# Optimization experiments

Measured on AMD Instinct MI355X. Metric: run time of the kernel, lower is better.

The kernel has to match this reference:

```python
import jax, jax.numpy as jnp
import numpy as np

K, N, E, D = 4, 2048, 4096, 128
BETA = 0.6
EPS = 0.01           # epsilon in hard-sigmoid gating
LAM = 0.05           # lambda_schedule
TC0, TCMAX = 0.3, 0.7
COS_EPS = 1e-8       # F.cosine_similarity eps
MAX_SCORED_EDGES = 500
EDGE_DENSITY = 0.008


def setup_inputs() -> dict:
    key = jax.random.key(0)
    ks = jax.random.split(key, 8)
    s = 0.02
    H = (jax.random.uniform(ks[0], (K, N, E)) < EDGE_DENSITY).astype(jnp.float32)
    X = jax.random.normal(ks[1], (N, D), jnp.float32)
    return dict(
        H=H, X=X, epoch=50,
        mlp_w1=jax.random.normal(ks[2], (K, D, D), jnp.float32) * s,
        mlp_b1=jnp.zeros((K, D), jnp.float32),
        mlp_w2=jax.random.normal(ks[3], (K, D, D), jnp.float32) * s,
        mlp_b2=jnp.zeros((K, D), jnp.float32),
        comp_W=jax.random.normal(ks[4], (K, D, D), jnp.float32) * 0.01,
        att_w1=jax.random.normal(ks[5], (K, D, D // 2), jnp.float32) * s,
        att_b1=jnp.zeros((K, D // 2), jnp.float32),
        att_w2=jax.random.normal(ks[6], (K, D // 2, 1), jnp.float32) * s,
        att_b2=jnp.zeros((K, 1), jnp.float32),
    )


def reference(H, X, epoch, mlp_w1, mlp_b1, mlp_w2, mlp_b2, comp_W,
              att_w1, att_b1, att_w2, att_b2):
    # ---- component level (Eq. 4, batched over K) ----
    h1 = jax.nn.relu(jnp.einsum('nd,kdh->knh', X, mlp_w1) + mlp_b1[:, None, :])
    Xk = jnp.einsum('knh,khe->kne', h1, mlp_w2) + mlp_b2[:, None, :]        # [K,N,D]
    a1 = jax.nn.relu(jnp.einsum('knd,kdh->knh', Xk, att_w1) + att_b1[:, None, :])
    att = jax.nn.sigmoid(jnp.einsum('knh,kho->kno', a1, att_w2) + att_b2[:, None, :])
    S_att = att.mean(axis=(1, 2))                                            # [K]
    frob = jnp.sqrt((comp_W ** 2).sum(axis=(1, 2)))                          # ||W_k||_F
    featn = jnp.sqrt((Xk ** 2).sum(axis=(1, 2)))                             # ||MLP(X_k)||_2 (Frobenius)
    imp = BETA * frob * featn + (1.0 - BETA) * S_att
    pi_c = jax.nn.softmax(imp)
    theta_c = TC0 + (1.0 - jnp.exp(-LAM * epoch)) * (TCMAX - TC0)            # Eq. 3 schedule
    gates = jnp.clip((pi_c - theta_c) / EPS + 0.5, 0.0, 1.0)                 # hard sigmoid
    # K_min = max(1, int(0.1*K)) = 1 -> force top-1 gate open
    keep = jax.nn.one_hot(jnp.argmax(gates), K, dtype=gates.dtype)
    gates = jnp.maximum(gates, keep)

    xnorm = jnp.linalg.norm(X, axis=1)                                       # [N]
    xhat = X / jnp.maximum(xnorm, COS_EPS)[:, None]
    er = jnp.arange(E)
    eye = jnp.eye(N, dtype=bool)

    Hp_l, eg_l, npi_l = [], [], []
    for k in range(K):  # small fixed component count
        Hk = H[k]
        mask = Hk > 0                                                        # [N,E]
        cnt = mask.sum(axis=0)                                               # nodes per hyperedge
        order = jnp.cumsum(mask, axis=0)
        i = jnp.argmax(mask, axis=0)                                         # first incident node
        j = jnp.argmax(mask & (order == 2), axis=0)                          # second incident node
        cos = (xhat[i] * xhat[j]).sum(-1)                                    # [E]
        A = Hk[i, er] * Hk[j, er]                                            # A_ij per edge
        # torch loop: only first 500 edges scored; <2-node edges get 0.1; rest 0
        imp_e = jnp.where(er < MAX_SCORED_EDGES,
                          jnp.where(cnt >= 2, A * cos, 0.1), 0.0)
        pi_e = jax.nn.softmax(imp_e)
        theta_e = jnp.minimum(theta_c, pi_e.mean() + jnp.std(pi_e, ddof=1))  # torch.std unbiased
        eg = jnp.clip((pi_e - theta_e) / EPS + 0.5, 0.0, 1.0)
        eg = jnp.where((eg.sum() < 1.0) & (er == jnp.argmax(pi_e)), 1.0, eg)
        eg_eff = jnp.where(gates[k] > 0.5, eg, jnp.ones_like(eg))
        Hp = Hk * gates[k] * eg_eff[None, :]                                 # pruned incidence

        # ---- node level (Eq. 7) on pruned graph ----
        B = (Hp > 0).astype(Hk.dtype)
        Adj = ((B @ B.T) > 0) & (~eye)                                       # shared-hyperedge neighbors
        degf = Adj.sum(axis=1).astype(Hk.dtype)
        nsum = Adj.astype(Hk.dtype) @ xhat                                   # sum of neighbor unit vecs
        avg = jnp.where(degf > 0, (xhat * nsum).sum(-1) / jnp.maximum(degf, 1.0), 0.0)
        npi = jax.nn.softmax(avg * xnorm)
        Hp_l.append(Hp); eg_l.append(eg); npi_l.append(npi)

    return (jnp.stack(Hp_l), gates, jnp.stack(eg_l), jnp.stack(npi_l))
```

## Files before the change

### kernel.cpp

```cpp
#include <hip/hip_runtime.h>
#include <math.h>

#define KCOMP 4
#define NN 2048
#define EE 4096
#define DD 128
#define MAXNE 96
#define MAXSE 500
#define BETA_C 0.6f
#define EPS_G 0.01f
#define LAM_S 0.05f
#define TC0_C 0.3f
#define TCMAX_C 0.7f
#define COS_EPS_C 1e-8f

typedef float vf4 __attribute__((ext_vector_type(4)));

static const size_t OFF_XHAT   = 0;
static const size_t OFF_XNORM  = 1048576;
static const size_t OFF_SCAL   = 1056768;
static const size_t OFF_NCNT   = 1057024;
static const size_t OFF_EMASK  = 1089792;
static const size_t OFF_NELIST = 5284096;
static const size_t OFF_IMPE   = 6856960;
static const size_t OFF_EGS    = 6865152;
static const size_t OFF_Z      = 6930688;
static const size_t OFF_FEAT   = 6963456;
static const size_t OFF_ATT    = 6965504;
static const size_t OFF_FROB   = 6967552;

__global__ __launch_bounds__(1024) void k_d1(
    const float4* __restrict__ H4, unsigned* __restrict__ emask,
    const float* __restrict__ X, float* __restrict__ xhat, float* __restrict__ xnorm,
    const float* __restrict__ w1, const float* __restrict__ b1,
    const float* __restrict__ w2, const float* __restrict__ b2,
    const float* __restrict__ aw1, const float* __restrict__ ab1,
    const float* __restrict__ aw2, const float* __restrict__ ab2,
    const float4* __restrict__ compW4, int* __restrict__ ncnt,
    unsigned short* __restrict__ nelist,
    float* __restrict__ featA, float* __restrict__ attA, float* __restrict__ frobA) {
  __shared__ float smem[16416];
  int b = blockIdx.x, t = threadIdx.x;
  if (b < 128) {
    int k = b >> 5;
    int bx = b & 31;
    float* Xs  = smem;
    float* H1s = smem + 8192;
    float* A1s = H1s;
    float* red = smem + 16384;
    int n0 = bx * 64;
    for (int i = t; i < 64 * 128; i += 1024) Xs[i] = X[(size_t)n0 * 128 + i];
    __syncthreads();

    int h = t & 127, g = t >> 7;
    const float* W1 = w1 + (size_t)k * 128 * 128;
    float acc[8];
    {
      float bb = b1[k * 128 + h];
#pragma unroll
      for (int rr = 0; rr < 8; ++rr) acc[rr] = bb;
    }
    for (int d = 0; d < 128; d += 4) {
      float wa = W1[(d + 0) * 128 + h];
      float wb = W1[(d + 1) * 128 + h];
      float wc = W1[(d + 2) * 128 + h];
      float wd2 = W1[(d + 3) * 128 + h];
#pragma unroll
      for (int rr = 0; rr < 8; ++rr) {
        float4 x = *(const float4*)&Xs[(g * 8 + rr) * 128 + d];
        acc[rr] = fmaf(x.x, wa, acc[rr]); acc[rr] = fmaf(x.y, wb, acc[rr]);
        acc[rr] = fmaf(x.z, wc, acc[rr]); acc[rr] = fmaf(x.w, wd2, acc[rr]);
      }
    }
#pragma unroll
    for (int rr = 0; rr < 8; ++rr) H1s[(g * 8 + rr) * 128 + h] = fmaxf(acc[rr], 0.f);
    __syncthreads();

    const float* W2 = w2 + (size_t)k * 128 * 128;
    {
      float bb = b2[k * 128 + h];
#pragma unroll
      for (int rr = 0; rr < 8; ++rr) acc[rr] = bb;
    }
    for (int d = 0; d < 128; d += 4) {
      float wa = W2[(d + 0) * 128 + h];
      float wb = W2[(d + 1) * 128 + h];
      float wc = W2[(d + 2) * 128 + h];
      float wd2 = W2[(d + 3) * 128 + h];
#pragma unroll
      for (int rr = 0; rr < 8; ++rr) {
        float4 x = *(const float4*)&H1s[(g * 8 + rr) * 128 + d];
        acc[rr] = fmaf(x.x, wa, acc[rr]); acc[rr] = fmaf(x.y, wb, acc[rr]);
        acc[rr] = fmaf(x.z, wc, acc[rr]); acc[rr] = fmaf(x.w, wd2, acc[rr]);
      }
    }
    float fpart = 0.f;
    __syncthreads();
#pragma unroll
    for (int rr = 0; rr < 8; ++rr) {
      Xs[(g * 8 + rr) * 128 + h] = acc[rr];
      fpart = fmaf(acc[rr], acc[rr], fpart);
    }
    __syncthreads();

    int h2 = t & 63, g4 = t >> 6;
    const float* AW1 = aw1 + (size_t)k * 128 * 64;
    float a4[4];
    {
      float ab = ab1[k * 64 + h2];
#pragma unroll
      for (int q = 0; q < 4; ++q) a4[q] = ab;
    }
    for (int d = 0; d < 128; d += 4) {
      float wa = AW1[(d + 0) * 64 + h2];
      float wb = AW1[(d + 1) * 64 + h2];
      float wc = AW1[(d + 2) * 64 + h2];
      float wd2 = AW1[(d + 3) * 64 + h2];
#pragma unroll
      for (int q = 0; q < 4; ++q) {
        float4 x = *(const float4*)&Xs[(g4 * 4 + q) * 128 + d];
        a4[q] = fmaf(x.x, wa, a4[q]); a4[q] = fmaf(x.y, wb, a4[q]);
        a4[q] = fmaf(x.z, wc, a4[q]); a4[q] = fmaf(x.w, wd2, a4[q]);
      }
    }
    __syncthreads();
#pragma unroll
    for (int q = 0; q < 4; ++q) A1s[(g4 * 4 + q) * 64 + h2] = fmaxf(a4[q], 0.f);
    __syncthreads();

    float attsum = 0.f;
    if (t < 64) {
      const float* AW2 = aw2 + (size_t)k * 64;
      float a = ab2[k];
      for (int d = 0; d < 64; d += 4) {
        float4 av = *(const float4*)&A1s[t * 64 + d];
        a = fmaf(av.x, AW2[d + 0], a);
        a = fmaf(av.y, AW2[d + 1], a);
        a = fmaf(av.z, AW2[d + 2], a);
        a = fmaf(av.w, AW2[d + 3], a);
      }
      attsum = 1.f / (1.f + expf(-a));
    }
    for (int o = 32; o > 0; o >>= 1) {
      fpart  += __shfl_xor(fpart, o, 64);
      attsum += __shfl_xor(attsum, o, 64);
    }
    int wv = t >> 6, ln = t & 63;
    if (ln == 0) { red[wv] = fpart; red[16 + wv] = attsum; }
    __syncthreads();
    if (t == 0) {
      float fs = 0.f, as = 0.f;
#pragma unroll
      for (int i = 0; i < 16; i++) { fs += red[i]; as += red[16 + i]; }
      featA[k * 128 + bx] = fs;
      attA[k * 128 + bx]  = as;
    }
    return;
  }
  if (b < 384) {
    unsigned* lds = (unsigned*)smem;
    int sb = b - 128;
    int k = sb >> 6;
    int rem = sb & 63;
    int ch_super = rem >> 4;
    int e4_super = rem & 15;
    int chi = t >> 6;
    int e4i = t & 63;
    int ch = ch_super * 16 + chi;
    int e4 = e4_super * 64 + e4i;
    int n0 = ch * 32;
    const float4* p = H4 + ((size_t)(k * NN + n0)) * (EE / 4) + e4;
    unsigned w0 = 0, w1b = 0, w2b = 0, w3 = 0;
    for (int rb = 0; rb < 32; rb += 8) {
      float4 v[8];
#pragma unroll
      for (int u = 0; u < 8; ++u) v[u] = p[(size_t)(rb + u) * (EE / 4)];
#pragma unroll
      for (int u = 0; u < 8; ++u) {
        unsigned bit = 1u << (rb + u);
        w0  |= (v[u].x > 0.f) ? bit : 0u;
        w1b |= (v[u].y > 0.f) ? bit : 0u;
        w2b |= (v[u].z > 0.f) ? bit : 0u;
        w3  |= (v[u].w > 0.f) ? bit : 0u;
      }
    }
    int el = e4i * 4;
    lds[(el + 0) * 17 + chi] = w0;
    lds[(el + 1) * 17 + chi] = w1b;
    lds[(el + 2) * 17 + chi] = w2b;
    lds[(el + 3) * 17 + chi] = w3;
    {
      int ebase = e4 * 4;
      unsigned ws[4] = {w0, w1b, w2b, w3};
#pragma unroll
      for (int j = 0; j < 4; ++j) {
        unsigned wd = ws[j];
        while (wd) {
          int bit = __builtin_ctz(wd); wd &= wd - 1;
          int node = n0 + bit;
          int slot = atomicAdd(&ncnt[k * NN + node], 1);
          if (slot < MAXNE)
            nelist[((size_t)(k * NN + node)) * MAXNE + slot] =
                (unsigned short)(ebase + j);
        }
      }
    }
    __syncthreads();
    int e_base = e4_super * 256;
    int wi = t & 15;
    int eo = t >> 4;
#pragma unroll
    for (int it = 0; it < 4; ++it) {
      int e_local = it * 64 + eo;
      emask[((size_t)(k * EE) + e_base + e_local) * 64 + ch_super * 16 + wi] =
          lds[e_local * 17 + wi];
    }
    return;
  }
  if (b < 512) {
    int xb = b - 384;
    int node = xb * 16 + (t >> 6);
    int lane = t & 63;
    float2 v = ((const float2*)X)[(size_t)node * 64 + lane];
    float ss = v.x * v.x + v.y * v.y;
    for (int o = 32; o > 0; o >>= 1) ss += __shfl_xor(ss, o, 64);
    float nrm = sqrtf(ss);
    float den = fmaxf(nrm, COS_EPS_C);
    if (lane == 0) xnorm[node] = nrm;
    float2 o2; o2.x = v.x / den; o2.y = v.y / den;
    ((float2*)xhat)[(size_t)node * 64 + lane] = o2;
    return;
  }
  {
    int fb = b - 512;
    int k = fb >> 2, idx = fb & 3;
    float* red = smem;
    float4 v = compW4[(size_t)k * 4096 + idx * 1024 + t];
    float s = v.x * v.x + v.y * v.y + v.z * v.z + v.w * v.w;
    for (int o = 32; o > 0; o >>= 1) s += __shfl_xor(s, o, 64);
    int wv = t >> 6, ln = t & 63;
    if (ln == 0) red[wv] = s;
    __syncthreads();
    if (t == 0) {
      float fs = 0.f;
#pragma unroll
      for (int i = 0; i < 16; i++) fs += red[i];
      frobA[k * 4 + idx] = fs;
    }
  }
}

__global__ void k_d2(const unsigned* __restrict__ emask, const float* __restrict__ xhat,
                     float* __restrict__ impE) {
  int t = threadIdx.x;
  int k = blockIdx.y;
  int bx = blockIdx.x;
  int e = bx * 4 + (t >> 6);
  int lane = t & 63;
  unsigned w = emask[((size_t)(k * EE) + e) * 64 + lane];
  int pc = __popc(w);
  for (int o = 32; o > 0; o >>= 1) pc += __shfl_xor(pc, o, 64);
  float impv = 0.1f;
  if (pc >= 2) {
    unsigned l1 = w ? (unsigned)((lane << 5) + __builtin_ctz(w)) : 0xffffffffu;
    unsigned wr = w & (w - 1);
    unsigned l2 = wr ? (unsigned)((lane << 5) + __builtin_ctz(wr)) : 0xffffffffu;
    unsigned g1 = l1;
    for (int o = 32; o > 0; o >>= 1) {
      unsigned x = (unsigned)__shfl_xor((int)g1, o, 64);
      g1 = g1 < x ? g1 : x;
    }
    unsigned cand = (l1 == g1) ? l2 : l1;
    unsigned g2 = cand;
    for (int o = 32; o > 0; o >>= 1) {
      unsigned x = (unsigned)__shfl_xor((int)g2, o, 64);
      g2 = g2 < x ? g2 : x;
    }
    float2 xi = ((const float2*)xhat)[(size_t)g1 * 64 + lane];
    float2 xj = ((const float2*)xhat)[(size_t)g2 * 64 + lane];
    float d = xi.x * xj.x + xi.y * xj.y;
    for (int o = 32; o > 0; o >>= 1) d += __shfl_xor(d, o, 64);
    impv = d;
  }
  if (lane == 0) impE[k * 512 + e] = impv;
}

__device__ __forceinline__ float blockReduceSum16(float v, float* red, int t) {
  for (int o = 32; o > 0; o >>= 1) v += __shfl_xor(v, o, 64);
  __syncthreads();
  if ((t & 63) == 0) red[t >> 6] = v;
  __syncthreads();
  float s = red[0];
#pragma unroll
  for (int i = 1; i < 16; i++) s += red[i];
  return s;
}

__global__ void k_edgegate(const float* __restrict__ impE,
                           const float* __restrict__ featA, const float* __restrict__ attA,
                           const float* __restrict__ frobA, float* __restrict__ scal,
                           const int* __restrict__ epoch, float* __restrict__ out_gates,
                           float* __restrict__ egscaled, float* __restrict__ out_eg) {
  __shared__ float red[16];
  __shared__ int redi[16];
  __shared__ float imps[KCOMP];
  int k = blockIdx.x;
  int t = threadIdx.x;
  int wv0 = t >> 6, ln0 = t & 63;
  if (wv0 < KCOMP) {
    float pf = (ln0 < 32) ? featA[wv0 * 128 + ln0] : 0.f;
    float pa = (ln0 < 32) ? attA[wv0 * 128 + ln0] : 0.f;
    float pr = (ln0 < 4) ? frobA[wv0 * 4 + ln0] : 0.f;
    for (int o = 32; o > 0; o >>= 1) {
      pf += __shfl_xor(pf, o, 64);
      pa += __shfl_xor(pa, o, 64);
      pr += __shfl_xor(pr, o, 64);
    }
    if (ln0 == 0)
      imps[wv0] = BETA_C * sqrtf(pr) * sqrtf(pf) + (1.f - BETA_C) * (pa / (float)NN);
  }
  __syncthreads();
  float gates[KCOMP];
  float tc;
  {
    float mx = imps[0];
    for (int kk = 1; kk < KCOMP; kk++) mx = fmaxf(mx, imps[kk]);
    float ex[KCOMP], ssum = 0.f;
    for (int kk = 0; kk < KCOMP; kk++) { ex[kk] = expf(imps[kk] - mx); ssum += ex[kk]; }
    tc = TC0_C + (1.f - expf(-LAM_S * (float)epoch[0])) * (TCMAX_C - TC0_C);
    for (int kk = 0; kk < KCOMP; kk++) {
      float pi = ex[kk] / ssum;
      gates[kk] = fminf(fmaxf((pi - tc) / EPS_G + 0.5f, 0.f), 1.f);
    }
    int am = 0; float bv2 = gates[0];
    for (int kk = 1; kk < KCOMP; kk++) if (gates[kk] > bv2) { bv2 = gates[kk]; am = kk; }
    gates[am] = fmaxf(gates[am], 1.f);
  }
  if (t == 0) {
    scal[12 + k] = gates[k];
    if (k == 0) for (int kk = 0; kk < KCOMP; kk++) out_gates[kk] = gates[kk];
  }
  float imp[4];
#pragma unroll
  for (int j = 0; j < 4; j++) {
    int e = t + j * 1024;
    imp[j] = (e < MAXSE) ? impE[k * 512 + e] : 0.f;
  }
  float m = fmaxf(fmaxf(imp[0], imp[1]), fmaxf(imp[2], imp[3]));
  for (int o = 32; o > 0; o >>= 1) m = fmaxf(m, __shfl_xor(m, o, 64));
  __syncthreads();
  if ((t & 63) == 0) red[t >> 6] = m;
  __syncthreads();
  m = red[0];
#pragma unroll
  for (int i = 1; i < 16; i++) m = fmaxf(m, red[i]);
  float p[4], psum = 0.f;
#pragma unroll
  for (int j = 0; j < 4; j++) { p[j] = expf(imp[j] - m); psum += p[j]; }
  float S = blockReduceSum16(psum, red, t);
  float pi[4], tot = 0.f;
#pragma unroll
  for (int j = 0; j < 4; j++) { pi[j] = p[j] / S; tot += pi[j]; }
  float T = blockReduceSum16(tot, red, t);
  float mean = T / (float)EE;
  float devs = 0.f;
#pragma unroll
  for (int j = 0; j < 4; j++) { float d = pi[j] - mean; devs = fmaf(d, d, devs); }
  float V = blockReduceSum16(devs, red, t);
  float stdv = sqrtf(V / (float)(EE - 1));
  float theta = fminf(tc, mean + stdv);
  float eg[4], egsum = 0.f;
#pragma unroll
  for (int j = 0; j < 4; j++) {
    eg[j] = fminf(fmaxf((pi[j] - theta) / EPS_G + 0.5f, 0.f), 1.f);
    egsum += eg[j];
  }
  float EGS = blockReduceSum16(egsum, red, t);
  float bv = -1e30f; int bi = 0x7fffffff;
#pragma unroll
  for (int j = 0; j < 4; j++) if (pi[j] > bv) { bv = pi[j]; bi = t + j * 1024; }
  for (int o = 32; o > 0; o >>= 1) {
    float ov = __shfl_xor(bv, o, 64); int oi = __shfl_xor(bi, o, 64);
    if (ov > bv || (ov == bv && oi < bi)) { bv = ov; bi = oi; }
  }
  __syncthreads();
  if ((t & 63) == 0) { red[t >> 6] = bv; redi[t >> 6] = bi; }
  __syncthreads();
  float abv = red[0]; int abi = redi[0];
#pragma unroll
  for (int i = 1; i < 16; i++) {
    float ov = red[i]; int oi = redi[i];
    if (ov > abv || (ov == abv && oi < abi)) { abv = ov; abi = oi; }
  }
  float g = gates[k];
#pragma unroll
  for (int j = 0; j < 4; j++) {
    int e = t + j * 1024;
    float egv = eg[j];
    if (EGS < 1.f && e == abi) egv = 1.f;
    out_eg[(size_t)k * EE + e] = egv;
    float eff = (g > 0.5f) ? egv : 1.f;
    egscaled[k * EE + e] = g * eff;
  }
}

__global__ void k_hprow(const unsigned* __restrict__ emask,
                        const int* __restrict__ ncnt, const unsigned short* __restrict__ nelist,
                        const float* __restrict__ egs, const float* __restrict__ scal,
                        const float* __restrict__ xhat, const float* __restrict__ xnorm,
                        float* __restrict__ out, float* __restrict__ z) {
  __shared__ unsigned short elds[MAXNE];
  __shared__ float evals[MAXNE];
  __shared__ unsigned wpart[4][64];
  __shared__ unsigned short list[2048];
  __shared__ int cnt_s;
  __shared__ float sred[4];
  int k = blockIdx.y, n = blockIdx.x, t = threadIdx.x;
  float g = scal[12 + k];
  float* orow = out + ((size_t)(k * NN + n)) * EE;
  vf4* o4 = (vf4*)orow;
  vf4 z4 = {0.f, 0.f, 0.f, 0.f};
  if (g <= 0.f) {
#pragma unroll
    for (int i = 0; i < 4; i++) __builtin_nontemporal_store(z4, &o4[t + i * 256]);
    if (t == 0) z[k * NN + n] = 0.f;
    return;
  }
  int ec = ncnt[k * NN + n]; if (ec > MAXNE) ec = MAXNE;
  if (t == 0) cnt_s = 0;
  if (t < ec) {
    int e = nelist[((size_t)(k * NN + n)) * MAXNE + t];
    elds[t] = (unsigned short)e;
    evals[t] = egs[k * EE + e];
  }
#pragma unroll
  for (int i = 0; i < 4; i++) __builtin_nontemporal_store(z4, &o4[t + i * 256]);
  __syncthreads();
  if (t < ec) orow[elds[t]] = evals[t];
  int lane = t & 63, wv = t >> 6;
  unsigned acc = 0;
  for (int it = wv; it < ec; it += 4) {
    if (evals[it] > 0.f) acc |= emask[((size_t)(k * EE) + elds[it]) * 64 + lane];
  }
  wpart[wv][lane] = acc;
  __syncthreads();
  if (t < 64) {
    unsigned w = wpart[0][t] | wpart[1][t] | wpart[2][t] | wpart[3][t];
    if (t == (n >> 5)) w &= ~(1u << (n & 31));
    int c = __popc(w);
    if (c > 0) {
      int base = atomicAdd(&cnt_s, c);
      while (w) {
        int b = __builtin_ctz(w); w &= w - 1;
        list[base++] = (unsigned short)((t << 5) + b);
      }
    }
  }
  __syncthreads();
  int cnt = cnt_s;
  if (cnt == 0) { if (t == 0) z[k * NN + n] = 0.f; return; }
  int fc = lane & 31, hh = lane >> 5;
  float4 xn4 = ((const float4*)xhat)[(size_t)n * 32 + fc];
  float a = 0.f;
#pragma unroll 4
  for (int it = wv * 2 + hh; it < cnt; it += 8) {
    int m = (int)list[it];
    float4 xm = ((const float4*)xhat)[(size_t)m * 32 + fc];
    a += xn4.x * xm.x + xn4.y * xm.y + xn4.z * xm.z + xn4.w * xm.w;
  }
  for (int o = 32; o > 0; o >>= 1) a += __shfl_xor(a, o, 64);
  if (lane == 0) sred[wv] = a;
  __syncthreads();
  if (t == 0) {
    float s = sred[0] + sred[1] + sred[2] + sred[3];
    z[k * NN + n] = (s / (float)cnt) * xnorm[n];
  }
}

__global__ void k_npi(const float* __restrict__ z, float* __restrict__ out_npi) {
  __shared__ float red[4];
  int k = blockIdx.x, t = threadIdx.x;
  float v[8]; float m = -1e30f;
#pragma unroll
  for (int j = 0; j < 8; j++) { v[j] = z[k * NN + t + j * 256]; m = fmaxf(m, v[j]); }
  for (int o = 32; o > 0; o >>= 1) m = fmaxf(m, __shfl_xor(m, o, 64));
  if ((t & 63) == 0) red[t >> 6] = m;
  __syncthreads();
  m = fmaxf(fmaxf(red[0], red[1]), fmaxf(red[2], red[3]));
  __syncthreads();
  float pe[8]; float s = 0.f;
#pragma unroll
  for (int j = 0; j < 8; j++) { pe[j] = expf(v[j] - m); s += pe[j]; }
  for (int o = 32; o > 0; o >>= 1) s += __shfl_xor(s, o, 64);
  if ((t & 63) == 0) red[t >> 6] = s;
  __syncthreads();
  s = red[0] + red[1] + red[2] + red[3];
#pragma unroll
  for (int j = 0; j < 8; j++) out_npi[k * NN + t + j * 256] = pe[j] / s;
}

extern "C" void kernel_launch(void* const* d_in, const int* in_sizes, int n_in,
                              void* d_out, int out_size, void* d_ws, size_t ws_size,
                              hipStream_t stream) {
  const float* H     = (const float*)d_in[0];
  const float* X     = (const float*)d_in[1];
  const int*   epoch = (const int*)d_in[2];
  const float* w1    = (const float*)d_in[3];
  const float* b1    = (const float*)d_in[4];
  const float* w2    = (const float*)d_in[5];
  const float* b2    = (const float*)d_in[6];
  const float* compW = (const float*)d_in[7];
  const float* aw1   = (const float*)d_in[8];
  const float* ab1   = (const float*)d_in[9];
  const float* aw2   = (const float*)d_in[10];
  const float* ab2   = (const float*)d_in[11];

  char* ws = (char*)d_ws;
  float* xhat  = (float*)(ws + OFF_XHAT);
  float* xnorm = (float*)(ws + OFF_XNORM);
  float* scal  = (float*)(ws + OFF_SCAL);
  int*   ncnt  = (int*)(ws + OFF_NCNT);
  unsigned* emask = (unsigned*)(ws + OFF_EMASK);
  unsigned short* nelist = (unsigned short*)(ws + OFF_NELIST);
  float* impE  = (float*)(ws + OFF_IMPE);
  float* egs   = (float*)(ws + OFF_EGS);
  float* zbuf  = (float*)(ws + OFF_Z);
  float* featA = (float*)(ws + OFF_FEAT);
  float* attA  = (float*)(ws + OFF_ATT);
  float* frobA = (float*)(ws + OFF_FROB);

  float* out       = (float*)d_out;
  float* out_gates = out + (size_t)KCOMP * NN * EE;
  float* out_eg    = out_gates + KCOMP;
  float* out_npi   = out_eg + (size_t)KCOMP * EE;

  hipMemsetAsync(ncnt, 0, (size_t)KCOMP * NN * sizeof(int), stream);
  k_d1<<<528, 1024, 0, stream>>>((const float4*)H, emask, X, xhat, xnorm,
                                 w1, b1, w2, b2, aw1, ab1, aw2, ab2,
                                 (const float4*)compW, ncnt, nelist, featA, attA, frobA);
  k_d2<<<dim3(125, KCOMP), 256, 0, stream>>>(emask, xhat, impE);
  k_edgegate<<<KCOMP, 1024, 0, stream>>>(impE, featA, attA, frobA, scal, epoch,
                                         out_gates, egs, out_eg);
  k_hprow<<<dim3(NN, KCOMP), 256, 0, stream>>>(emask, ncnt, nelist, egs, scal, xhat, xnorm,
                                               out, zbuf);
  k_npi<<<KCOMP, 256, 0, stream>>>(zbuf, out_npi);
}
```

Before: 299.2 us.

## Register-tile MLP matmuls in k_d1 and fold edge scoring into k_edgegate

The per-component MLP and attention matmuls in k_d1 now use 2x4 and 1x4 register tiles with float4 weight and shared-memory loads, in place of one output column per thread. This raises arithmetic per load and cuts LDS traffic. The separate k_d2 launch that scored the first 500 hyperedges is removed, and that work now runs at the start of k_edgegate into shared memory. This saves one kernel launch and a global round trip, but the scoring now runs on only 4 blocks instead of 500.

```diff
diff --git a/kernel.cpp b/kernel.cpp
--- a/kernel.cpp
+++ b/kernel.cpp
@@ -22,7 +22,6 @@
 static const size_t OFF_NCNT   = 1057024;
 static const size_t OFF_EMASK  = 1089792;
 static const size_t OFF_NELIST = 5284096;
-static const size_t OFF_IMPE   = 6856960;
 static const size_t OFF_EGS    = 6865152;
 static const size_t OFF_Z      = 6930688;
 static const size_t OFF_FEAT   = 6963456;
@@ -52,80 +51,122 @@
     for (int i = t; i < 64 * 128; i += 1024) Xs[i] = X[(size_t)n0 * 128 + i];
     __syncthreads();
 
-    int h = t & 127, g = t >> 7;
+    int hq = t & 31, rq = t >> 5;
+    int h0 = hq * 4;
+    float acc0[4], acc1[4];
+    {
+      float4 bb = *(const float4*)&b1[k * 128 + h0];
+      acc0[0] = bb.x; acc0[1] = bb.y; acc0[2] = bb.z; acc0[3] = bb.w;
+      acc1[0] = bb.x; acc1[1] = bb.y; acc1[2] = bb.z; acc1[3] = bb.w;
+    }
     const float* W1 = w1 + (size_t)k * 128 * 128;
-    float acc[8];
-    {
-      float bb = b1[k * 128 + h];
-#pragma unroll
-      for (int rr = 0; rr < 8; ++rr) acc[rr] = bb;
-    }
     for (int d = 0; d < 128; d += 4) {
-      float wa = W1[(d + 0) * 128 + h];
-      float wb = W1[(d + 1) * 128 + h];
-      float wc = W1[(d + 2) * 128 + h];
-      float wd2 = W1[(d + 3) * 128 + h];
-#pragma unroll
-      for (int rr = 0; rr < 8; ++rr) {
-        float4 x = *(const float4*)&Xs[(g * 8 + rr) * 128 + d];
-        acc[rr] = fmaf(x.x, wa, acc[rr]); acc[rr] = fmaf(x.y, wb, acc[rr]);
-        acc[rr] = fmaf(x.z, wc, acc[rr]); acc[rr] = fmaf(x.w, wd2, acc[rr]);
-      }
-    }
-#pragma unroll
-    for (int rr = 0; rr < 8; ++rr) H1s[(g * 8 + rr) * 128 + h] = fmaxf(acc[rr], 0.f);
-    __syncthreads();
-
+      float wm[4][4], xa0[4], xa1[4];
+#pragma unroll
+      for (int i = 0; i < 4; ++i) {
+        float4 w = *(const float4*)&W1[(d + i) * 128 + h0];
+        wm[i][0] = w.x; wm[i][1] = w.y; wm[i][2] = w.z; wm[i][3] = w.w;
+      }
+      {
+        float4 x0 = *(const float4*)&Xs[(rq * 2 + 0) * 128 + d];
+        float4 x1 = *(const float4*)&Xs[(rq * 2 + 1) * 128 + d];
+        xa0[0] = x0.x; xa0[1] = x0.y; xa0[2] = x0.z; xa0[3] = x0.w;
+        xa1[0] = x1.x; xa1[1] = x1.y; xa1[2] = x1.z; xa1[3] = x1.w;
+      }
+#pragma unroll
+      for (int j = 0; j < 4; ++j) {
+#pragma unroll
+        for (int i = 0; i < 4; ++i) acc0[j] = fmaf(xa0[i], wm[i][j], acc0[j]);
+#pragma unroll
+        for (int i = 0; i < 4; ++i) acc1[j] = fmaf(xa1[i], wm[i][j], acc1[j]);
+      }
+    }
+    {
+      float4 s0, s1;
+      s0.x = fmaxf(acc0[0], 0.f); s0.y = fmaxf(acc0[1], 0.f);
+      s0.z = fmaxf(acc0[2], 0.f); s0.w = fmaxf(acc0[3], 0.f);
+      s1.x = fmaxf(acc1[0], 0.f); s1.y = fmaxf(acc1[1], 0.f);
+      s1.z = fmaxf(acc1[2], 0.f); s1.w = fmaxf(acc1[3], 0.f);
+      *(float4*)&H1s[(rq * 2 + 0) * 128 + h0] = s0;
+      *(float4*)&H1s[(rq * 2 + 1) * 128 + h0] = s1;
+    }
+    __syncthreads();
+
+    {
+      float4 bb = *(const float4*)&b2[k * 128 + h0];
+      acc0[0] = bb.x; acc0[1] = bb.y; acc0[2] = bb.z; acc0[3] = bb.w;
+      acc1[0] = bb.x; acc1[1] = bb.y; acc1[2] = bb.z; acc1[3] = bb.w;
+    }
     const float* W2 = w2 + (size_t)k * 128 * 128;
-    {
-      float bb = b2[k * 128 + h];
-#pragma unroll
-      for (int rr = 0; rr < 8; ++rr) acc[rr] = bb;
-    }
     for (int d = 0; d < 128; d += 4) {
-      float wa = W2[(d + 0) * 128 + h];
-      float wb = W2[(d + 1) * 128 + h];
-      float wc = W2[(d + 2) * 128 + h];
-      float wd2 = W2[(d + 3) * 128 + h];
-#pragma unroll
-      for (int rr = 0; rr < 8; ++rr) {
-        float4 x = *(const float4*)&H1s[(g * 8 + rr) * 128 + d];
-        acc[rr] = fmaf(x.x, wa, acc[rr]); acc[rr] = fmaf(x.y, wb, acc[rr]);
-        acc[rr] = fmaf(x.z, wc, acc[rr]); acc[rr] = fmaf(x.w, wd2, acc[rr]);
+      float wm[4][4], xa0[4], xa1[4];
+#pragma unroll
+      for (int i = 0; i < 4; ++i) {
+        float4 w = *(const float4*)&W2[(d + i) * 128 + h0];
+        wm[i][0] = w.x; wm[i][1] = w.y; wm[i][2] = w.z; wm[i][3] = w.w;
+      }
+      {
+        float4 x0 = *(const float4*)&H1s[(rq * 2 + 0) * 128 + d];
+        float4 x1 = *(const float4*)&H1s[(rq * 2 + 1) * 128 + d];
+        xa0[0] = x0.x; xa0[1] = x0.y; xa0[2] = x0.z; xa0[3] = x0.w;
+        xa1[0] = x1.x; xa1[1] = x1.y; xa1[2] = x1.z; xa1[3] = x1.w;
+      }
+#pragma unroll
+      for (int j = 0; j < 4; ++j) {
+#pragma unroll
+        for (int i = 0; i < 4; ++i) acc0[j] = fmaf(xa0[i], wm[i][j], acc0[j]);
+#pragma unroll
+        for (int i = 0; i < 4; ++i) acc1[j] = fmaf(xa1[i], wm[i][j], acc1[j]);
       }
     }
     float fpart = 0.f;
     __syncthreads();
-#pragma unroll
-    for (int rr = 0; rr < 8; ++rr) {
-      Xs[(g * 8 + rr) * 128 + h] = acc[rr];
-      fpart = fmaf(acc[rr], acc[rr], fpart);
-    }
-    __syncthreads();
-
-    int h2 = t & 63, g4 = t >> 6;
+    {
+      float4 s0, s1;
+      s0.x = acc0[0]; s0.y = acc0[1]; s0.z = acc0[2]; s0.w = acc0[3];
+      s1.x = acc1[0]; s1.y = acc1[1]; s1.z = acc1[2]; s1.w = acc1[3];
+      *(float4*)&Xs[(rq * 2 + 0) * 128 + h0] = s0;
+      *(float4*)&Xs[(rq * 2 + 1) * 128 + h0] = s1;
+#pragma unroll
+      for (int j = 0; j < 4; ++j) {
+        fpart = fmaf(acc0[j], acc0[j], fpart);
+        fpart = fmaf(acc1[j], acc1[j], fpart);
+      }
+    }
+    __syncthreads();
+
+    int hq3 = t & 15, rq3 = t >> 4;
+    int h0a = hq3 * 4;
     const float* AW1 = aw1 + (size_t)k * 128 * 64;
     float a4[4];
     {
-      float ab = ab1[k * 64 + h2];
-#pragma unroll
-      for (int q = 0; q < 4; ++q) a4[q] = ab;
+      float4 ab = *(const float4*)&ab1[k * 64 + h0a];
+      a4[0] = ab.x; a4[1] = ab.y; a4[2] = ab.z; a4[3] = ab.w;
     }
     for (int d = 0; d < 128; d += 4) {
-      float wa = AW1[(d + 0) * 64 + h2];
-      float wb = AW1[(d + 1) * 64 + h2];
-      float wc = AW1[(d + 2) * 64 + h2];
-      float wd2 = AW1[(d + 3) * 64 + h2];
-#pragma unroll
-      for (int q = 0; q < 4; ++q) {
-        float4 x = *(const float4*)&Xs[(g4 * 4 + q) * 128 + d];
-        a4[q] = fmaf(x.x, wa, a4[q]); a4[q] = fmaf(x.y, wb, a4[q]);
-        a4[q] = fmaf(x.z, wc, a4[q]); a4[q] = fmaf(x.w, wd2, a4[q]);
-      }
-    }
-    __syncthreads();
-#pragma unroll
-    for (int q = 0; q < 4; ++q) A1s[(g4 * 4 + q) * 64 + h2] = fmaxf(a4[q], 0.f);
+      float wm[4][4], xa[4];
+#pragma unroll
+      for (int i = 0; i < 4; ++i) {
+        float4 w = *(const float4*)&AW1[(d + i) * 64 + h0a];
+        wm[i][0] = w.x; wm[i][1] = w.y; wm[i][2] = w.z; wm[i][3] = w.w;
+      }
+      {
+        float4 x = *(const float4*)&Xs[rq3 * 128 + d];
+        xa[0] = x.x; xa[1] = x.y; xa[2] = x.z; xa[3] = x.w;
+      }
+#pragma unroll
+      for (int j = 0; j < 4; ++j) {
+#pragma unroll
+        for (int i = 0; i < 4; ++i) a4[j] = fmaf(xa[i], wm[i][j], a4[j]);
+      }
+    }
+    __syncthreads();
+    {
+      float4 s;
+      s.x = fmaxf(a4[0], 0.f); s.y = fmaxf(a4[1], 0.f);
+      s.z = fmaxf(a4[2], 0.f); s.w = fmaxf(a4[3], 0.f);
+      *(float4*)&A1s[rq3 * 64 + h0a] = s;
+    }
     __syncthreads();
 
     float attsum = 0.f;
@@ -250,41 +291,6 @@
   }
 }
 
-__global__ void k_d2(const unsigned* __restrict__ emask, const float* __restrict__ xhat,
-                     float* __restrict__ impE) {
-  int t = threadIdx.x;
-  int k = blockIdx.y;
-  int bx = blockIdx.x;
-  int e = bx * 4 + (t >> 6);
-  int lane = t & 63;
-  unsigned w = emask[((size_t)(k * EE) + e) * 64 + lane];
-  int pc = __popc(w);
-  for (int o = 32; o > 0; o >>= 1) pc += __shfl_xor(pc, o, 64);
-  float impv = 0.1f;
-  if (pc >= 2) {
-    unsigned l1 = w ? (unsigned)((lane << 5) + __builtin_ctz(w)) : 0xffffffffu;
-    unsigned wr = w & (w - 1);
-    unsigned l2 = wr ? (unsigned)((lane << 5) + __builtin_ctz(wr)) : 0xffffffffu;
-    unsigned g1 = l1;
-    for (int o = 32; o > 0; o >>= 1) {
-      unsigned x = (unsigned)__shfl_xor((int)g1, o, 64);
-      g1 = g1 < x ? g1 : x;
-    }
-    unsigned cand = (l1 == g1) ? l2 : l1;
-    unsigned g2 = cand;
-    for (int o = 32; o > 0; o >>= 1) {
-      unsigned x = (unsigned)__shfl_xor((int)g2, o, 64);
-      g2 = g2 < x ? g2 : x;
-    }
-    float2 xi = ((const float2*)xhat)[(size_t)g1 * 64 + lane];
-    float2 xj = ((const float2*)xhat)[(size_t)g2 * 64 + lane];
-    float d = xi.x * xj.x + xi.y * xj.y;
-    for (int o = 32; o > 0; o >>= 1) d += __shfl_xor(d, o, 64);
-    impv = d;
-  }
-  if (lane == 0) impE[k * 512 + e] = impv;
-}
-
 __device__ __forceinline__ float blockReduceSum16(float v, float* red, int t) {
   for (int o = 32; o > 0; o >>= 1) v += __shfl_xor(v, o, 64);
   __syncthreads();
@@ -296,17 +302,46 @@
   return s;
 }
 
-__global__ void k_edgegate(const float* __restrict__ impE,
+__global__ void k_edgegate(const unsigned* __restrict__ emask, const float* __restrict__ xhat,
                            const float* __restrict__ featA, const float* __restrict__ attA,
                            const float* __restrict__ frobA, float* __restrict__ scal,
                            const int* __restrict__ epoch, float* __restrict__ out_gates,
                            float* __restrict__ egscaled, float* __restrict__ out_eg) {
+  __shared__ float impsE[MAXSE];
   __shared__ float red[16];
   __shared__ int redi[16];
   __shared__ float imps[KCOMP];
   int k = blockIdx.x;
   int t = threadIdx.x;
   int wv0 = t >> 6, ln0 = t & 63;
+  for (int e = wv0; e < MAXSE; e += 16) {
+    unsigned w = emask[((size_t)(k * EE) + e) * 64 + ln0];
+    int pc = __popc(w);
+    for (int o = 32; o > 0; o >>= 1) pc += __shfl_xor(pc, o, 64);
+    float impv = 0.1f;
+    if (pc >= 2) {
+      unsigned l1 = w ? (unsigned)((ln0 << 5) + __builtin_ctz(w)) : 0xffffffffu;
+      unsigned wr = w & (w - 1);
+      unsigned l2 = wr ? (unsigned)((ln0 << 5) + __builtin_ctz(wr)) : 0xffffffffu;
+      unsigned g1 = l1;
+      for (int o = 32; o > 0; o >>= 1) {
+        unsigned x = (unsigned)__shfl_xor((int)g1, o, 64);
+        g1 = g1 < x ? g1 : x;
+      }
+      unsigned cand = (l1 == g1) ? l2 : l1;
+      unsigned g2 = cand;
+      for (int o = 32; o > 0; o >>= 1) {
+        unsigned x = (unsigned)__shfl_xor((int)g2, o, 64);
+        g2 = g2 < x ? g2 : x;
+      }
+      float2 xi = ((const float2*)xhat)[(size_t)g1 * 64 + ln0];
+      float2 xj = ((const float2*)xhat)[(size_t)g2 * 64 + ln0];
+      float d = xi.x * xj.x + xi.y * xj.y;
+      for (int o = 32; o > 0; o >>= 1) d += __shfl_xor(d, o, 64);
+      impv = d;
+    }
+    if (ln0 == 0) impsE[e] = impv;
+  }
   if (wv0 < KCOMP) {
     float pf = (ln0 < 32) ? featA[wv0 * 128 + ln0] : 0.f;
     float pa = (ln0 < 32) ? attA[wv0 * 128 + ln0] : 0.f;
@@ -344,7 +379,7 @@
 #pragma unroll
   for (int j = 0; j < 4; j++) {
     int e = t + j * 1024;
-    imp[j] = (e < MAXSE) ? impE[k * 512 + e] : 0.f;
+    imp[j] = (e < MAXSE) ? impsE[e] : 0.f;
   }
   float m = fmaxf(fmaxf(imp[0], imp[1]), fmaxf(imp[2], imp[3]));
   for (int o = 32; o > 0; o >>= 1) m = fmaxf(m, __shfl_xor(m, o, 64));
@@ -522,7 +557,6 @@
   int*   ncnt  = (int*)(ws + OFF_NCNT);
   unsigned* emask = (unsigned*)(ws + OFF_EMASK);
   unsigned short* nelist = (unsigned short*)(ws + OFF_NELIST);
-  float* impE  = (float*)(ws + OFF_IMPE);
   float* egs   = (float*)(ws + OFF_EGS);
   float* zbuf  = (float*)(ws + OFF_Z);
   float* featA = (float*)(ws + OFF_FEAT);
@@ -538,8 +572,7 @@
   k_d1<<<528, 1024, 0, stream>>>((const float4*)H, emask, X, xhat, xnorm,
                                  w1, b1, w2, b2, aw1, ab1, aw2, ab2,
                                  (const float4*)compW, ncnt, nelist, featA, attA, frobA);
-  k_d2<<<dim3(125, KCOMP), 256, 0, stream>>>(emask, xhat, impE);
-  k_edgegate<<<KCOMP, 1024, 0, stream>>>(impE, featA, attA, frobA, scal, epoch,
+  k_edgegate<<<KCOMP, 1024, 0, stream>>>(emask, xhat, featA, attA, frobA, scal, epoch,
                                          out_gates, egs, out_eg);
   k_hprow<<<dim3(NN, KCOMP), 256, 0, stream>>>(emask, ncnt, nelist, egs, scal, xhat, xnorm,
                                                out, zbuf);
```

After: 353.3 us. +18.1%, slower.
